# Performance work log

Hardware: AMD Instinct MI355X
Metric: run time of the kernel (lower is better)

The kernel has to match this reference:

```python
import jax, jax.numpy as jnp
import numpy as np

N_NODES, N_EDGES, N_FEAT, N_GRAPHS = 100_000, 1_600_000, 3, 512
FENG = jnp.array([4, 8, 9, 12, 13, 14])  # feng_filters(): second-order pairs with scale2 > scale1
LEAKY_SLOPE = 0.01


def _wavelet_constructor():
    # Psi_j = P^{2^{j-1}} - P^{2^j}, j = 1..4, over 17 diffusion levels P^0..P^16
    W = np.zeros((4, 17), dtype=np.float32)
    for j, (a, b) in enumerate([(1, 2), (2, 4), (4, 8), (8, 16)]):
        W[j, a] = 1.0
        W[j, b] = -1.0
    return jnp.asarray(W)


def _gcn_edges(edge_index, n):
    # gcn_norm with self-loops: w_ij = d_i^-1/2 d_j^-1/2 on A + I
    loop = jnp.arange(n)
    src = jnp.concatenate([edge_index[0], loop])
    dst = jnp.concatenate([edge_index[1], loop])
    deg = jax.ops.segment_sum(jnp.ones_like(dst, dtype=jnp.float32), dst, num_segments=n)
    dinv = jnp.where(deg > 0, jax.lax.rsqrt(deg), 0.0)
    w = dinv[src] * dinv[dst]
    return src, dst, w


def _diffuse(x, src, dst, w, n):
    # lazy random walk: 0.5 * (x + P_norm x), x: [N, C, k]
    agg = jax.ops.segment_sum(w[:, None, None] * x[src], dst, num_segments=n)
    return 0.5 * (x + agg)


def _scatter_features(x, edge_index):
    n, c = x.shape
    src, dst, w = _gcn_edges(edge_index, n)
    Wav = _wavelet_constructor()

    s0 = x[:, :, None]                                   # [N, C, 1]
    levels = [s0]
    for _ in range(16):
        levels.append(_diffuse(levels[-1], src, dst, w, n))
    D = jnp.stack(levels)                                # [17, N, C, 1]
    sub = jnp.einsum('wt,tnck->wnck', Wav, D)[..., 0]    # [4, N, C]
    s1 = jnp.abs(jnp.transpose(sub, (1, 2, 0)))          # [N, C, 4]

    levels2 = [s1]
    for _ in range(16):
        levels2.append(_diffuse(levels2[-1], src, dst, w, n))
    D2 = jnp.stack(levels2)                              # [17, N, C, 4]
    sub2 = jnp.einsum('wt,tncf->wncf', Wav, D2)          # [4, N, C, 4]
    # reproduce the exact torch transpose/reshape sequence of LEGS Scatter
    t = jnp.abs(jnp.transpose(sub2, (1, 0, 2, 3)).reshape(n, c, 16))  # [N, C, 16]
    s2 = jnp.swapaxes(t, 1, 2)[:, FENG]                  # [N, 6, C]

    xcat = jnp.concatenate([s0, s1], axis=2)             # [N, C, 5]
    xcat = jnp.swapaxes(xcat, 1, 2)                      # [N, 5, C]
    xcat = jnp.concatenate([xcat, s2], axis=1)           # [N, 11, C]
    return xcat.reshape(n, 11 * c)                       # [N, 33]


def _scatter_moments(x, batch, num_graphs):
    # per-graph mean / variance / skew (3 central moments), concatenated -> [G, 3*F]
    cnt = jax.ops.segment_sum(jnp.ones((x.shape[0],), x.dtype), batch, num_segments=num_graphs)
    cnt = jnp.maximum(cnt, 1.0)[:, None]
    mean = jax.ops.segment_sum(x, batch, num_segments=num_graphs) / cnt
    dev = x - mean[batch]
    var = jax.ops.segment_sum(dev * dev, batch, num_segments=num_graphs) / cnt
    skew = jax.ops.segment_sum(dev * dev * dev, batch, num_segments=num_graphs) / cnt
    return jnp.concatenate([mean, var, skew], axis=1)


def setup_inputs() -> dict:
    key = jax.random.key(0)
    ks = jax.random.split(key, 8)
    x = jax.random.normal(ks[0], (N_NODES, N_FEAT), dtype=jnp.float32)
    edge_index = jax.random.randint(ks[1], (2, N_EDGES), 0, N_NODES)
    batch = jnp.sort(jax.random.randint(ks[2], (N_NODES,), 0, N_GRAPHS))

    def lin(k, fan_in, fan_out):
        k1, k2 = jax.random.split(k)
        bound = 1.0 / np.sqrt(fan_in)
        W = jax.random.uniform(k1, (fan_in, fan_out), minval=-bound, maxval=bound, dtype=jnp.float32)
        b = jax.random.uniform(k2, (fan_out,), minval=-bound, maxval=bound, dtype=jnp.float32)
        return W, b

    W1, b1 = lin(ks[3], 99, 128)
    W2, b2 = lin(ks[4], 128, 64)
    W3, b3 = lin(ks[5], 64, 64)
    We, be = lin(ks[6], 64, 32)
    Wc, bc = lin(ks[7], 32, 1)
    return {"x": x, "W1": W1, "b1": b1, "W2": W2, "b2": b2, "W3": W3, "b3": b3,
            "We": We, "be": be, "Wc": Wc, "bc": bc,
            "edge_index": edge_index, "batch": batch, "num_graphs": N_GRAPHS}


def reference(x, W1, b1, W2, b2, W3, b3, We, be, Wc, bc, edge_index, batch, num_graphs):
    act = lambda v: jax.nn.leaky_relu(v, LEAKY_SLOPE)
    feats = _scatter_features(x, edge_index)              # [N, 33]
    h = _scatter_moments(feats, batch, num_graphs)        # [G, 99]
    h = act(h)
    h = act(h @ W1 + b1)        # dropout is identity (p=0.0)
    h = act(h @ W2 + b2)
    h = h @ W3 + b3             # no activation before embedding layer (as in source)
    embedding = h @ We + be
    output = embedding @ Wc + bc  # classifier applied to embedding (pre-activation)
    return embedding, output
```

## Files before the change

### kernel.cpp

```cpp
#include <hip/hip_runtime.h>

#define N_NODES 100000
#define N_EDGES 1600000
#define NG      512
#define NPART   8
#define NPP     12500
#define BCAP    245760
#define BQ      1024
#define BFLUSH  512
#define NBBLK   256
#define EPB     ((N_EDGES + NBBLK - 1) / NBBLK)

static __device__ __forceinline__ float lrelu(float v) {
    return v >= 0.0f ? v : 0.01f * v;
}

__global__ void k_zero_i32(int* __restrict__ p, int n) {
    int i = blockIdx.x * blockDim.x + threadIdx.x;
    if (i < n) p[i] = 0;
}

__global__ void k_copy_i32(const int* __restrict__ s, int* __restrict__ d, int n) {
    int i = blockIdx.x * blockDim.x + threadIdx.x;
    if (i < n) d[i] = s[i];
}

__global__ void k_dinv(const int* __restrict__ counts, float* __restrict__ dinv,
                       float* __restrict__ dinv2, float* __restrict__ sdeg) {
    int i = blockIdx.x * blockDim.x + threadIdx.x;
    if (i < N_NODES) {
        float deg = (float)(counts[i] + 1);
        float s = sqrtf(deg);
        sdeg[i] = s;
        dinv[i] = 1.0f / s;
        dinv2[i] = 1.0f / deg;
    }
}

__global__ __launch_bounds__(256) void k_bin(const int* __restrict__ esrc,
                                             const int* __restrict__ edst,
                                             int* __restrict__ gcur,
                                             uint2* __restrict__ gbuf) {
    __shared__ uint2 buf[NPART][BQ];
    __shared__ int lcnt[NPART];
    __shared__ int gbase[NPART];
    if (threadIdx.x < NPART) lcnt[threadIdx.x] = 0;
    __syncthreads();
    int base = blockIdx.x * EPB;
    int end = base + EPB; if (end > N_EDGES) end = N_EDGES;
    for (int r = base; r < end; r += 2048) {
        int rend = r + 2048; if (rend > end) rend = end;
        for (int e = r + (int)threadIdx.x; e < rend; e += 256) {
            int d = edst[e];
            int s = esrc[e];
            int b = d / NPP;
            int pos = atomicAdd(&lcnt[b], 1);
            if (pos < BQ) {
                buf[b][pos] = make_uint2((unsigned)s, (unsigned)d);
            } else {
                int g = atomicAdd(&gcur[b], 1);
                gbuf[(size_t)b * BCAP + g] = make_uint2((unsigned)s, (unsigned)d);
            }
        }
        __syncthreads();
        for (int b = 0; b < NPART; ++b) {
            int cnt = lcnt[b];
            if (cnt >= BFLUSH) {
                if (threadIdx.x == 0) gbase[b] = atomicAdd(&gcur[b], BFLUSH);
                __syncthreads();
                int gb = gbase[b];
                for (int i = threadIdx.x; i < BFLUSH; i += 256)
                    gbuf[(size_t)b * BCAP + gb + i] = buf[b][i];
                __syncthreads();
                int inb = cnt < BQ ? cnt : BQ;
                int rem = inb - BFLUSH;
                for (int i = threadIdx.x; i < rem; i += 256)
                    buf[b][i] = buf[b][BFLUSH + i];
                __syncthreads();
                if (threadIdx.x == 0) lcnt[b] = rem;
                __syncthreads();
            }
        }
    }
    for (int b = 0; b < NPART; ++b) {
        int cnt = lcnt[b]; if (cnt > BQ) cnt = BQ;
        if (cnt > 0) {
            if (threadIdx.x == 0) gbase[b] = atomicAdd(&gcur[b], cnt);
            __syncthreads();
            int gb = gbase[b];
            for (int i = threadIdx.x; i < cnt; i += 256)
                gbuf[(size_t)b * BCAP + gb + i] = buf[b][i];
        }
        __syncthreads();
    }
}

__global__ __launch_bounds__(1024) void k_count_b(const int* __restrict__ gcur,
                                                  const uint2* __restrict__ gbuf,
                                                  int* __restrict__ counts) {
    __shared__ int h[NPP];
    int p = blockIdx.x & (NPART - 1);
    int slice = blockIdx.x >> 3;
    for (int i = threadIdx.x; i < NPP; i += 1024) h[i] = 0;
    __syncthreads();
    int n = gcur[p];
    int per = (n + 7) / 8;
    int lo = slice * per, hi = lo + per; if (hi > n) hi = n;
    const uint2* bb = gbuf + (size_t)p * BCAP;
    int pl = p * NPP;
    for (int i = lo + (int)threadIdx.x; i < hi; i += 1024) {
        int d = (int)bb[i].y - pl;
        atomicAdd(&h[d], 1);
    }
    __syncthreads();
    for (int i = threadIdx.x; i < NPP; i += 1024)
        if (h[i]) atomicAdd(&counts[pl + i], h[i]);
}

__global__ void k_scan_block(const int* __restrict__ counts, int* __restrict__ offsets,
                             int* __restrict__ bsums, int n) {
    __shared__ int tmp[1024];
    int gid = blockIdx.x * 1024 + threadIdx.x;
    int v = (gid < n) ? counts[gid] : 0;
    tmp[threadIdx.x] = v;
    __syncthreads();
    for (int off = 1; off < 1024; off <<= 1) {
        int t = (threadIdx.x >= off) ? tmp[threadIdx.x - off] : 0;
        __syncthreads();
        tmp[threadIdx.x] += t;
        __syncthreads();
    }
    if (gid < n) offsets[gid + 1] = tmp[threadIdx.x];
    if (threadIdx.x == 1023) bsums[blockIdx.x] = tmp[1023];
}

__global__ void k_scan_bsums(int* __restrict__ bsums, int nb) {
    if (blockIdx.x == 0 && threadIdx.x == 0) {
        int acc = 0;
        for (int b = 0; b < nb; ++b) { int v = bsums[b]; bsums[b] = acc; acc += v; }
    }
}

__global__ void k_scan_add(int* __restrict__ offsets, const int* __restrict__ bsums, int n) {
    int gid = blockIdx.x * 1024 + threadIdx.x;
    if (gid < n) offsets[gid + 1] += bsums[blockIdx.x];
    if (gid == 0) offsets[0] = 0;
}

__global__ __launch_bounds__(256) void k_scatter_b(const int* __restrict__ gcur,
                                                   const uint2* __restrict__ gbuf,
                                                   int* __restrict__ cursor,
                                                   int* __restrict__ csr_src) {
    int p = blockIdx.x & (NPART - 1);
    int slice = blockIdx.x >> 3;
    int n = gcur[p];
    int per = (n + 15) / 16;
    int lo = slice * per, hi = lo + per; if (hi > n) hi = n;
    const uint2* bb = gbuf + (size_t)p * BCAP;
    for (int i = lo + (int)threadIdx.x; i < hi; i += 256) {
        uint2 e = bb[i];
        int pos = atomicAdd(&cursor[e.y], 1);
        csr_src[pos] = (int)e.x;
    }
}

__global__ void k_vinit(const float* __restrict__ x, const float* __restrict__ dinv,
                        float4* __restrict__ v) {
    int i = blockIdx.x * blockDim.x + threadIdx.x;
    if (i >= N_NODES) return;
    float di = dinv[i];
    v[i] = make_float4(di * x[i * 3 + 0], di * x[i * 3 + 1], di * x[i * 3 + 2], 0.0f);
}

__global__ __launch_bounds__(256) void k_vdiff3(
    const float4* __restrict__ xin, float4* __restrict__ xout,
    const int* __restrict__ offs, const int* __restrict__ csrc,
    const float* __restrict__ dinv2) {
    int t = blockIdx.x * 256 + threadIdx.x;
    if (t >= N_NODES * 8) return;
    int h = t & 7;
    int i = t >> 3;
    int b = offs[i], e = offs[i + 1];
    float a0 = 0.0f, a1 = 0.0f, a2 = 0.0f;
    for (int p = b + h; p < e; p += 8) {
        int s = csrc[p];
        float4 xv = xin[s];
        a0 += xv.x; a1 += xv.y; a2 += xv.z;
    }
    a0 += __shfl_xor(a0, 1, 64); a1 += __shfl_xor(a1, 1, 64); a2 += __shfl_xor(a2, 1, 64);
    a0 += __shfl_xor(a0, 2, 64); a1 += __shfl_xor(a1, 2, 64); a2 += __shfl_xor(a2, 2, 64);
    a0 += __shfl_xor(a0, 4, 64); a1 += __shfl_xor(a1, 4, 64); a2 += __shfl_xor(a2, 4, 64);
    if (h == 0) {
        float d2 = dinv2[i];
        float4 sv = xin[i];
        xout[i] = make_float4(0.5f * (sv.x + d2 * (a0 + sv.x)),
                              0.5f * (sv.y + d2 * (a1 + sv.y)),
                              0.5f * (sv.z + d2 * (a2 + sv.z)), 0.0f);
    }
}

__global__ __launch_bounds__(256) void k_vdiff12(
    const float4* __restrict__ xin, float4* __restrict__ xout,
    const int* __restrict__ offs, const int* __restrict__ csrc,
    const float* __restrict__ dinv2) {
    int t = blockIdx.x * 256 + threadIdx.x;
    if (t >= N_NODES * 12) return;
    int i = t / 12;
    int r = t % 12;
    int q = r >> 2;
    int h = r & 3;
    int b = offs[i], e = offs[i + 1];
    float ax = 0.0f, ay = 0.0f, az = 0.0f, aw = 0.0f;
    for (int p = b + h; p < e; p += 4) {
        int s = csrc[p];
        float4 xv = xin[s * 3 + q];
        ax += xv.x; ay += xv.y; az += xv.z; aw += xv.w;
    }
    ax += __shfl_xor(ax, 1, 64); ay += __shfl_xor(ay, 1, 64);
    az += __shfl_xor(az, 1, 64); aw += __shfl_xor(aw, 1, 64);
    ax += __shfl_xor(ax, 2, 64); ay += __shfl_xor(ay, 2, 64);
    az += __shfl_xor(az, 2, 64); aw += __shfl_xor(aw, 2, 64);
    if (h == 0) {
        float d2 = dinv2[i];
        float4 sv = xin[i * 3 + q];
        xout[i * 3 + q] = make_float4(0.5f * (sv.x + d2 * (ax + sv.x)),
                                      0.5f * (sv.y + d2 * (ay + sv.y)),
                                      0.5f * (sv.z + d2 * (az + sv.z)),
                                      0.5f * (sv.w + d2 * (aw + sv.w)));
    }
}

__global__ void k_s1v(const float4* __restrict__ L1, const float4* __restrict__ L2,
                      const float4* __restrict__ L4, const float4* __restrict__ L8,
                      const float4* __restrict__ L16, float* __restrict__ s1v) {
    int i = blockIdx.x * blockDim.x + threadIdx.x;
    if (i >= N_NODES) return;
    float4 v[5];
    v[0] = L1[i]; v[1] = L2[i]; v[2] = L4[i]; v[3] = L8[i]; v[4] = L16[i];
    float* out = s1v + (size_t)i * 12;
#pragma unroll
    for (int f = 0; f < 4; ++f) {
        out[0 * 4 + f] = fabsf(v[f].x - v[f + 1].x);
        out[1 * 4 + f] = fabsf(v[f].y - v[f + 1].y);
        out[2 * 4 + f] = fabsf(v[f].z - v[f + 1].z);
    }
}

__global__ void k_feats(const float* __restrict__ x, const float* __restrict__ s1v,
                        const float* __restrict__ M1, const float* __restrict__ M2,
                        const float* __restrict__ M4, const float* __restrict__ M8,
                        const float* __restrict__ M16, const float* __restrict__ sdeg,
                        float* __restrict__ feats) {
    int i = blockIdx.x * blockDim.x + threadIdx.x;
    if (i >= N_NODES) return;
    float sd = sdeg[i];
    float* out = feats + (size_t)i * 33;
    out[0] = x[i * 3 + 0];
    out[1] = x[i * 3 + 1];
    out[2] = x[i * 3 + 2];
    for (int r = 1; r <= 4; ++r)
        for (int c = 0; c < 3; ++c)
            out[r * 3 + c] = sd * s1v[(size_t)i * 12 + c * 4 + (r - 1)];
    const float* Ms[5] = {M1, M2, M4, M8, M16};
    const int FENG[6] = {4, 8, 9, 12, 13, 14};
    for (int m = 0; m < 6; ++m) {
        for (int c2 = 0; c2 < 3; ++c2) {
            int idx = c2 * 16 + FENG[m];
            int w = idx / 12, rem = idx % 12, cc = rem / 4, f = rem % 4;
            float v = Ms[w][(size_t)i * 12 + cc * 4 + f] - Ms[w + 1][(size_t)i * 12 + cc * 4 + f];
            out[(5 + m) * 3 + c2] = fabsf(sd * v);
        }
    }
}

static __device__ __forceinline__ int lower_bound_i(const int* __restrict__ a, int n, int key) {
    int lo = 0, hi = n;
    while (lo < hi) { int mid = (lo + hi) >> 1; if (a[mid] < key) lo = mid + 1; else hi = mid; }
    return lo;
}

__global__ __launch_bounds__(256) void k_moments_mean(
    const float* __restrict__ feats, const int* __restrict__ batch,
    float* __restrict__ meanbuf) {
    __shared__ float part[4][33];
    int g = blockIdx.x;
    int lo = lower_bound_i(batch, N_NODES, g);
    int hi = lower_bound_i(batch, N_NODES, g + 1);
    float acc[33];
#pragma unroll
    for (int c = 0; c < 33; ++c) acc[c] = 0.0f;
    for (int i = lo + (int)threadIdx.x; i < hi; i += 256) {
        const float* f = feats + (size_t)i * 33;
#pragma unroll
        for (int c = 0; c < 33; ++c) acc[c] += f[c];
    }
#pragma unroll
    for (int c = 0; c < 33; ++c) {
        float v = acc[c];
        for (int o = 32; o >= 1; o >>= 1) v += __shfl_down(v, o, 64);
        acc[c] = v;
    }
    int wid = threadIdx.x >> 6, lane = threadIdx.x & 63;
    if (lane == 0)
        for (int c = 0; c < 33; ++c) part[wid][c] = acc[c];
    __syncthreads();
    if (threadIdx.x < 33) {
        float cnt = (float)((hi - lo) > 1 ? (hi - lo) : 1);
        float s = part[0][threadIdx.x] + part[1][threadIdx.x] +
                  part[2][threadIdx.x] + part[3][threadIdx.x];
        meanbuf[g * 33 + threadIdx.x] = s / cnt;
    }
}

__global__ __launch_bounds__(256) void k_moments_vs(
    const float* __restrict__ feats, const int* __restrict__ batch,
    const float* __restrict__ meanbuf, float* __restrict__ h0) {
    __shared__ float part2[4][33];
    __shared__ float part3[4][33];
    int g = blockIdx.x;
    int lo = lower_bound_i(batch, N_NODES, g);
    int hi = lower_bound_i(batch, N_NODES, g + 1);
    float mu[33], a2[33], a3[33];
#pragma unroll
    for (int c = 0; c < 33; ++c) { mu[c] = meanbuf[g * 33 + c]; a2[c] = 0.0f; a3[c] = 0.0f; }
    for (int i = lo + (int)threadIdx.x; i < hi; i += 256) {
        const float* f = feats + (size_t)i * 33;
#pragma unroll
        for (int c = 0; c < 33; ++c) {
            float d = f[c] - mu[c];
            float d2 = d * d;
            a2[c] += d2;
            a3[c] += d2 * d;
        }
    }
#pragma unroll
    for (int c = 0; c < 33; ++c) {
        float v2 = a2[c], v3 = a3[c];
        for (int o = 32; o >= 1; o >>= 1) {
            v2 += __shfl_down(v2, o, 64);
            v3 += __shfl_down(v3, o, 64);
        }
        a2[c] = v2; a3[c] = v3;
    }
    int wid = threadIdx.x >> 6, lane = threadIdx.x & 63;
    if (lane == 0)
        for (int c = 0; c < 33; ++c) { part2[wid][c] = a2[c]; part3[wid][c] = a3[c]; }
    __syncthreads();
    if (threadIdx.x < 33) {
        int c = threadIdx.x;
        float cnt = (float)((hi - lo) > 1 ? (hi - lo) : 1);
        float v2 = part2[0][c] + part2[1][c] + part2[2][c] + part2[3][c];
        float v3 = part3[0][c] + part3[1][c] + part3[2][c] + part3[3][c];
        h0[g * 99 + c]      = lrelu(mu[c]);
        h0[g * 99 + 33 + c] = lrelu(v2 / cnt);
        h0[g * 99 + 66 + c] = lrelu(v3 / cnt);
    }
}

__global__ __launch_bounds__(128) void k_mlp(
    const float* __restrict__ h0,
    const float* __restrict__ W1, const float* __restrict__ b1,
    const float* __restrict__ W2, const float* __restrict__ b2,
    const float* __restrict__ W3, const float* __restrict__ b3,
    const float* __restrict__ We, const float* __restrict__ be,
    const float* __restrict__ Wc, const float* __restrict__ bc,
    float* __restrict__ emb, float* __restrict__ outp) {
    __shared__ float s0[99], s1[128], s2[64], s3[64], s4[32];
    int g = blockIdx.x;
    int t = threadIdx.x;
    if (t < 99) s0[t] = h0[g * 99 + t];
    __syncthreads();
    {
        float a = b1[t];
        for (int k = 0; k < 99; ++k) a += s0[k] * W1[k * 128 + t];
        s1[t] = lrelu(a);
    }
    __syncthreads();
    if (t < 64) {
        float a = b2[t];
        for (int k = 0; k < 128; ++k) a += s1[k] * W2[k * 64 + t];
        s2[t] = lrelu(a);
    }
    __syncthreads();
    if (t < 64) {
        float a = b3[t];
        for (int k = 0; k < 64; ++k) a += s2[k] * W3[k * 64 + t];
        s3[t] = a;
    }
    __syncthreads();
    if (t < 32) {
        float a = be[t];
        for (int k = 0; k < 64; ++k) a += s3[k] * We[k * 32 + t];
        s4[t] = a;
        emb[g * 32 + t] = a;
    }
    __syncthreads();
    if (t == 0) {
        float a = bc[0];
        for (int k = 0; k < 32; ++k) a += s4[k] * Wc[k];
        outp[g] = a;
    }
}

extern "C" void kernel_launch(void* const* d_in, const int* in_sizes, int n_in,
                              void* d_out, int out_size, void* d_ws, size_t ws_size,
                              hipStream_t stream) {
    const float* x   = (const float*)d_in[0];
    const float* W1  = (const float*)d_in[1];
    const float* b1  = (const float*)d_in[2];
    const float* W2  = (const float*)d_in[3];
    const float* b2  = (const float*)d_in[4];
    const float* W3  = (const float*)d_in[5];
    const float* b3  = (const float*)d_in[6];
    const float* We  = (const float*)d_in[7];
    const float* be  = (const float*)d_in[8];
    const float* Wc  = (const float*)d_in[9];
    const float* bc  = (const float*)d_in[10];
    const int*   eix = (const int*)d_in[11];
    const int*   batch = (const int*)d_in[12];
    const int* esrc = eix;
    const int* edst = eix + N_EDGES;

    char* ws = (char*)d_ws;
    size_t off = 0;
    auto alloc = [&](size_t bytes) -> void* {
        void* p = ws + off;
        off = (off + bytes + 255) & ~(size_t)255;
        return p;
    };
    int*   counts  = (int*)alloc((size_t)N_NODES * 4);
    int*   offsets = (int*)alloc((size_t)(N_NODES + 1) * 4);
    int*   cursor  = (int*)alloc((size_t)N_NODES * 4);
    float* dinv    = (float*)alloc((size_t)N_NODES * 4);
    float* dinv2   = (float*)alloc((size_t)N_NODES * 4);
    float* sdeg    = (float*)alloc((size_t)N_NODES * 4);
    int*   bsums   = (int*)alloc(1024 * 4);
    int*   gcur    = (int*)alloc(NPART * 4);
    uint2* gbuf    = (uint2*)alloc((size_t)NPART * BCAP * 8);
    int*   csr_src = (int*)alloc((size_t)N_EDGES * 4);
    float4* v0     = (float4*)alloc((size_t)N_NODES * 16);
    float4* p1[7];
    for (int i = 0; i < 7; ++i) p1[i] = (float4*)alloc((size_t)N_NODES * 16);
    float* s1v = (float*)alloc((size_t)N_NODES * 12 * 4);
    float* p2[7];
    for (int i = 0; i < 7; ++i) p2[i] = (float*)alloc((size_t)N_NODES * 12 * 4);
    float* feats = (float*)alloc((size_t)N_NODES * 33 * 4);
    float* meanb = (float*)alloc((size_t)NG * 33 * 4);
    float* h0 = (float*)alloc((size_t)NG * 99 * 4);
    (void)ws_size; (void)in_sizes; (void)n_in; (void)out_size;

    const int TB = 256;
    const int gbN = (N_NODES + TB - 1) / TB;
    const int nbScan = (N_NODES + 1023) / 1024;

    hipLaunchKernelGGL(k_zero_i32, dim3(gbN), dim3(TB), 0, stream, counts, N_NODES);
    hipLaunchKernelGGL(k_zero_i32, dim3(1), dim3(TB), 0, stream, gcur, NPART);
    hipLaunchKernelGGL(k_bin, dim3(NBBLK), dim3(TB), 0, stream, esrc, edst, gcur, gbuf);
    hipLaunchKernelGGL(k_count_b, dim3(64), dim3(1024), 0, stream, gcur, gbuf, counts);
    hipLaunchKernelGGL(k_dinv, dim3(gbN), dim3(TB), 0, stream, counts, dinv, dinv2, sdeg);
    hipLaunchKernelGGL(k_scan_block, dim3(nbScan), dim3(1024), 0, stream, counts, offsets, bsums, N_NODES);
    hipLaunchKernelGGL(k_scan_bsums, dim3(1), dim3(1), 0, stream, bsums, nbScan);
    hipLaunchKernelGGL(k_scan_add, dim3(nbScan), dim3(1024), 0, stream, offsets, bsums, N_NODES);
    hipLaunchKernelGGL(k_copy_i32, dim3(gbN), dim3(TB), 0, stream, offsets, cursor, N_NODES);
    hipLaunchKernelGGL(k_scatter_b, dim3(128), dim3(TB), 0, stream, gcur, gbuf, cursor, csr_src);

    hipLaunchKernelGGL(k_vinit, dim3(gbN), dim3(TB), 0, stream, x, dinv, v0);

    const int saveT[5] = {1, 2, 4, 8, 16};

    const float4* prev = v0;
    float4* saves1[5];
    {
        int si = 0, sc = 0;
        const int gb = (N_NODES * 8 + TB - 1) / TB;
        for (int t = 1; t <= 16; ++t) {
            float4* outb;
            if (si < 5 && t == saveT[si]) { outb = p1[si]; saves1[si] = outb; ++si; }
            else { outb = p1[5 + sc]; sc ^= 1; }
            hipLaunchKernelGGL(k_vdiff3, dim3(gb), dim3(TB), 0, stream,
                               prev, outb, offsets, csr_src, dinv2);
            prev = outb;
        }
    }
    hipLaunchKernelGGL(k_s1v, dim3(gbN), dim3(TB), 0, stream,
                       saves1[0], saves1[1], saves1[2], saves1[3], saves1[4], s1v);

    float* saves2[5];
    {
        const float* prev2 = s1v;
        int si = 0, sc = 0;
        const int gb = (N_NODES * 12 + TB - 1) / TB;
        for (int t = 1; t <= 16; ++t) {
            float* outb;
            if (si < 5 && t == saveT[si]) { outb = p2[si]; saves2[si] = outb; ++si; }
            else { outb = p2[5 + sc]; sc ^= 1; }
            hipLaunchKernelGGL(k_vdiff12, dim3(gb), dim3(TB), 0, stream,
                               (const float4*)prev2, (float4*)outb, offsets, csr_src, dinv2);
            prev2 = outb;
        }
    }

    hipLaunchKernelGGL(k_feats, dim3(gbN), dim3(TB), 0, stream,
                       x, s1v, saves2[0], saves2[1], saves2[2], saves2[3], saves2[4], sdeg, feats);
    hipLaunchKernelGGL(k_moments_mean, dim3(NG), dim3(256), 0, stream, feats, batch, meanb);
    hipLaunchKernelGGL(k_moments_vs, dim3(NG), dim3(256), 0, stream, feats, batch, meanb, h0);

    float* emb  = (float*)d_out;
    float* outp = (float*)d_out + NG * 32;
    hipLaunchKernelGGL(k_mlp, dim3(NG), dim3(128), 0, stream,
                       h0, W1, b1, W2, b2, W3, b3, We, be, Wc, bc, emb, outp);
}
```

Before: 847.2 us.

## Restructure 12-channel diffusion threading, fuse moment kernels, widen CSR scatter grid

The 12-channel diffusion kernel now uses 8 lanes per node, each loading all three float4 chunks of a neighbour. Before, 12 lanes per node each read one chunk, so the csr_src index read is shared across all channels. The two-pass moments computation (mean, then centred second and third moments) becomes a single pass over raw power sums, with variance and skew formed algebraically. This can lose precision through cancellation. The CSR scatter kernel gets 128 slices per partition instead of 16 to raise parallelism in graph construction.

```diff
diff --git a/kernel.cpp b/kernel.cpp
--- a/kernel.cpp
+++ b/kernel.cpp
@@ -10,6 +10,7 @@
 #define BFLUSH  512
 #define NBBLK   256
 #define EPB     ((N_EDGES + NBBLK - 1) / NBBLK)
+#define SCAT_SLICES 128
 
 static __device__ __forceinline__ float lrelu(float v) {
     return v >= 0.0f ? v : 0.01f * v;
@@ -154,7 +155,7 @@
     int p = blockIdx.x & (NPART - 1);
     int slice = blockIdx.x >> 3;
     int n = gcur[p];
-    int per = (n + 15) / 16;
+    int per = (n + SCAT_SLICES - 1) / SCAT_SLICES;
     int lo = slice * per, hi = lo + per; if (hi > n) hi = n;
     const uint2* bb = gbuf + (size_t)p * BCAP;
     for (int i = lo + (int)threadIdx.x; i < hi; i += 256) {
@@ -204,29 +205,43 @@
     const int* __restrict__ offs, const int* __restrict__ csrc,
     const float* __restrict__ dinv2) {
     int t = blockIdx.x * 256 + threadIdx.x;
-    if (t >= N_NODES * 12) return;
-    int i = t / 12;
-    int r = t % 12;
-    int q = r >> 2;
-    int h = r & 3;
+    if (t >= N_NODES * 8) return;
+    int h = t & 7;
+    int i = t >> 3;
     int b = offs[i], e = offs[i + 1];
-    float ax = 0.0f, ay = 0.0f, az = 0.0f, aw = 0.0f;
-    for (int p = b + h; p < e; p += 4) {
+    float a[12];
+#pragma unroll
+    for (int c = 0; c < 12; ++c) a[c] = 0.0f;
+    for (int p = b + h; p < e; p += 8) {
         int s = csrc[p];
-        float4 xv = xin[s * 3 + q];
-        ax += xv.x; ay += xv.y; az += xv.z; aw += xv.w;
-    }
-    ax += __shfl_xor(ax, 1, 64); ay += __shfl_xor(ay, 1, 64);
-    az += __shfl_xor(az, 1, 64); aw += __shfl_xor(aw, 1, 64);
-    ax += __shfl_xor(ax, 2, 64); ay += __shfl_xor(ay, 2, 64);
-    az += __shfl_xor(az, 2, 64); aw += __shfl_xor(aw, 2, 64);
+        float4 b0 = xin[s * 3 + 0];
+        float4 b1 = xin[s * 3 + 1];
+        float4 b2 = xin[s * 3 + 2];
+        a[0] += b0.x; a[1] += b0.y; a[2]  += b0.z; a[3]  += b0.w;
+        a[4] += b1.x; a[5] += b1.y; a[6]  += b1.z; a[7]  += b1.w;
+        a[8] += b2.x; a[9] += b2.y; a[10] += b2.z; a[11] += b2.w;
+    }
+#pragma unroll
+    for (int c = 0; c < 12; ++c) {
+        a[c] += __shfl_xor(a[c], 1, 64);
+        a[c] += __shfl_xor(a[c], 2, 64);
+        a[c] += __shfl_xor(a[c], 4, 64);
+    }
     if (h == 0) {
         float d2 = dinv2[i];
-        float4 sv = xin[i * 3 + q];
-        xout[i * 3 + q] = make_float4(0.5f * (sv.x + d2 * (ax + sv.x)),
-                                      0.5f * (sv.y + d2 * (ay + sv.y)),
-                                      0.5f * (sv.z + d2 * (az + sv.z)),
-                                      0.5f * (sv.w + d2 * (aw + sv.w)));
+        float4 s0 = xin[i * 3 + 0], s1 = xin[i * 3 + 1], s2 = xin[i * 3 + 2];
+        xout[i * 3 + 0] = make_float4(0.5f * (s0.x + d2 * (a[0] + s0.x)),
+                                      0.5f * (s0.y + d2 * (a[1] + s0.y)),
+                                      0.5f * (s0.z + d2 * (a[2] + s0.z)),
+                                      0.5f * (s0.w + d2 * (a[3] + s0.w)));
+        xout[i * 3 + 1] = make_float4(0.5f * (s1.x + d2 * (a[4] + s1.x)),
+                                      0.5f * (s1.y + d2 * (a[5] + s1.y)),
+                                      0.5f * (s1.z + d2 * (a[6] + s1.z)),
+                                      0.5f * (s1.w + d2 * (a[7] + s1.w)));
+        xout[i * 3 + 2] = make_float4(0.5f * (s2.x + d2 * (a[8] + s2.x)),
+                                      0.5f * (s2.y + d2 * (a[9] + s2.y)),
+                                      0.5f * (s2.z + d2 * (a[10] + s2.z)),
+                                      0.5f * (s2.w + d2 * (a[11] + s2.w)));
     }
 }
 
@@ -279,81 +294,40 @@
     return lo;
 }
 
-__global__ __launch_bounds__(256) void k_moments_mean(
+__global__ __launch_bounds__(256) void k_moments(
     const float* __restrict__ feats, const int* __restrict__ batch,
-    float* __restrict__ meanbuf) {
-    __shared__ float part[4][33];
+    float* __restrict__ h0) {
+    __shared__ float P1[4][33], P2[4][33], P3[4][33];
     int g = blockIdx.x;
     int lo = lower_bound_i(batch, N_NODES, g);
     int hi = lower_bound_i(batch, N_NODES, g + 1);
-    float acc[33];
-#pragma unroll
-    for (int c = 0; c < 33; ++c) acc[c] = 0.0f;
-    for (int i = lo + (int)threadIdx.x; i < hi; i += 256) {
-        const float* f = feats + (size_t)i * 33;
-#pragma unroll
-        for (int c = 0; c < 33; ++c) acc[c] += f[c];
-    }
-#pragma unroll
-    for (int c = 0; c < 33; ++c) {
-        float v = acc[c];
-        for (int o = 32; o >= 1; o >>= 1) v += __shfl_down(v, o, 64);
-        acc[c] = v;
-    }
-    int wid = threadIdx.x >> 6, lane = threadIdx.x & 63;
-    if (lane == 0)
-        for (int c = 0; c < 33; ++c) part[wid][c] = acc[c];
-    __syncthreads();
-    if (threadIdx.x < 33) {
-        float cnt = (float)((hi - lo) > 1 ? (hi - lo) : 1);
-        float s = part[0][threadIdx.x] + part[1][threadIdx.x] +
-                  part[2][threadIdx.x] + part[3][threadIdx.x];
-        meanbuf[g * 33 + threadIdx.x] = s / cnt;
-    }
-}
-
-__global__ __launch_bounds__(256) void k_moments_vs(
-    const float* __restrict__ feats, const int* __restrict__ batch,
-    const float* __restrict__ meanbuf, float* __restrict__ h0) {
-    __shared__ float part2[4][33];
-    __shared__ float part3[4][33];
-    int g = blockIdx.x;
-    int lo = lower_bound_i(batch, N_NODES, g);
-    int hi = lower_bound_i(batch, N_NODES, g + 1);
-    float mu[33], a2[33], a3[33];
-#pragma unroll
-    for (int c = 0; c < 33; ++c) { mu[c] = meanbuf[g * 33 + c]; a2[c] = 0.0f; a3[c] = 0.0f; }
-    for (int i = lo + (int)threadIdx.x; i < hi; i += 256) {
-        const float* f = feats + (size_t)i * 33;
-#pragma unroll
-        for (int c = 0; c < 33; ++c) {
-            float d = f[c] - mu[c];
-            float d2 = d * d;
-            a2[c] += d2;
-            a3[c] += d2 * d;
-        }
-    }
-#pragma unroll
-    for (int c = 0; c < 33; ++c) {
-        float v2 = a2[c], v3 = a3[c];
-        for (int o = 32; o >= 1; o >>= 1) {
-            v2 += __shfl_down(v2, o, 64);
-            v3 += __shfl_down(v3, o, 64);
-        }
-        a2[c] = v2; a3[c] = v3;
-    }
-    int wid = threadIdx.x >> 6, lane = threadIdx.x & 63;
-    if (lane == 0)
-        for (int c = 0; c < 33; ++c) { part2[wid][c] = a2[c]; part3[wid][c] = a3[c]; }
+    int w = threadIdx.x >> 6;
+    int l = threadIdx.x & 63;
+    float s1 = 0.0f, s2 = 0.0f, s3 = 0.0f;
+    if (l < 33) {
+        for (int i = lo + w; i < hi; i += 4) {
+            float v = feats[(size_t)i * 33 + l];
+            s1 += v;
+            s2 += v * v;
+            s3 += v * v * v;
+        }
+        P1[w][l] = s1; P2[w][l] = s2; P3[w][l] = s3;
+    }
     __syncthreads();
     if (threadIdx.x < 33) {
         int c = threadIdx.x;
+        float S1 = P1[0][c] + P1[1][c] + P1[2][c] + P1[3][c];
+        float S2 = P2[0][c] + P2[1][c] + P2[2][c] + P2[3][c];
+        float S3 = P3[0][c] + P3[1][c] + P3[2][c] + P3[3][c];
         float cnt = (float)((hi - lo) > 1 ? (hi - lo) : 1);
-        float v2 = part2[0][c] + part2[1][c] + part2[2][c] + part2[3][c];
-        float v3 = part3[0][c] + part3[1][c] + part3[2][c] + part3[3][c];
-        h0[g * 99 + c]      = lrelu(mu[c]);
-        h0[g * 99 + 33 + c] = lrelu(v2 / cnt);
-        h0[g * 99 + 66 + c] = lrelu(v3 / cnt);
+        float mu  = S1 / cnt;
+        float ex2 = S2 / cnt;
+        float ex3 = S3 / cnt;
+        float var = ex2 - mu * mu;
+        float skw = ex3 - 3.0f * mu * ex2 + 2.0f * mu * mu * mu;
+        h0[g * 99 + c]      = lrelu(mu);
+        h0[g * 99 + 33 + c] = lrelu(var);
+        h0[g * 99 + 66 + c] = lrelu(skw);
     }
 }
 
@@ -445,7 +419,6 @@
     float* p2[7];
     for (int i = 0; i < 7; ++i) p2[i] = (float*)alloc((size_t)N_NODES * 12 * 4);
     float* feats = (float*)alloc((size_t)N_NODES * 33 * 4);
-    float* meanb = (float*)alloc((size_t)NG * 33 * 4);
     float* h0 = (float*)alloc((size_t)NG * 99 * 4);
     (void)ws_size; (void)in_sizes; (void)n_in; (void)out_size;
 
@@ -462,7 +435,8 @@
     hipLaunchKernelGGL(k_scan_bsums, dim3(1), dim3(1), 0, stream, bsums, nbScan);
     hipLaunchKernelGGL(k_scan_add, dim3(nbScan), dim3(1024), 0, stream, offsets, bsums, N_NODES);
     hipLaunchKernelGGL(k_copy_i32, dim3(gbN), dim3(TB), 0, stream, offsets, cursor, N_NODES);
-    hipLaunchKernelGGL(k_scatter_b, dim3(128), dim3(TB), 0, stream, gcur, gbuf, cursor, csr_src);
+    hipLaunchKernelGGL(k_scatter_b, dim3(NPART * SCAT_SLICES), dim3(TB), 0, stream,
+                       gcur, gbuf, cursor, csr_src);
 
     hipLaunchKernelGGL(k_vinit, dim3(gbN), dim3(TB), 0, stream, x, dinv, v0);
 
@@ -489,7 +463,7 @@
     {
         const float* prev2 = s1v;
         int si = 0, sc = 0;
-        const int gb = (N_NODES * 12 + TB - 1) / TB;
+        const int gb = (N_NODES * 8 + TB - 1) / TB;
         for (int t = 1; t <= 16; ++t) {
             float* outb;
             if (si < 5 && t == saveT[si]) { outb = p2[si]; saves2[si] = outb; ++si; }
@@ -502,8 +476,7 @@
 
     hipLaunchKernelGGL(k_feats, dim3(gbN), dim3(TB), 0, stream,
                        x, s1v, saves2[0], saves2[1], saves2[2], saves2[3], saves2[4], sdeg, feats);
-    hipLaunchKernelGGL(k_moments_mean, dim3(NG), dim3(256), 0, stream, feats, batch, meanb);
-    hipLaunchKernelGGL(k_moments_vs, dim3(NG), dim3(256), 0, stream, feats, batch, meanb, h0);
+    hipLaunchKernelGGL(k_moments, dim3(NG), dim3(256), 0, stream, feats, batch, h0);
 
     float* emb  = (float*)d_out;
     float* outp = (float*)d_out + NG * 32;
```

Measured after the change: 809.4 us. -4.5%, faster.
